# Optimization experiments

Hardware: AMD Instinct MI355X
Metric: run time of the kernel (lower is better)

## Reference

```python
import jax, jax.numpy as jnp
import numpy as np

B = 4096       # batch of query embeddings
E = 512        # embedding_size
C = 2000       # num_classes
PROXIES = 32   # imprinted weight vectors per class
P = C * PROXIES  # 64000 total stacked weight rows
EPS = 1e-12    # torch F.normalize eps


def _l2_normalize(x):
    # F.normalize(x, p=2, dim=1): divide by norm clamped to eps
    n = jnp.linalg.norm(x, axis=1, keepdims=True)
    return x / jnp.maximum(n, EPS)


def setup_inputs() -> dict:
    key = jax.random.key(0)
    k1, k2 = jax.random.split(key)
    data = jax.random.normal(k1, (B, E), dtype=jnp.float32)
    w1 = jax.random.normal(k2, (P, E), dtype=jnp.float32)
    segment_ids = jnp.arange(P, dtype=jnp.int32)  # raw row index; class id derived in reference
    return {"data": data, "w1": w1, "segment_ids": segment_ids}


def reference(data, w1, segment_ids):
    # class id of each stacked weight row (contiguous blocks, as torch vstack([*w1s]))
    seg = (segment_ids * C) // P  # == idx // PROXIES, shape [P]
    # normalize: input data at forward time; weights were l2-normalized at imprint time
    d = _l2_normalize(data)   # [B, E]
    w = _l2_normalize(w1)     # [P, E]
    # x = w1 @ data.T : per-proxy activations  [P, B]
    x = jnp.einsum('pe,be->pb', w, d)
    # per-class max over each class's ragged proxy block -> [C, B]
    y = jax.ops.segment_max(x, seg, num_segments=C)
    return y
```

## Files before the change

kernel.cpp:

```cpp
#include <hip/hip_runtime.h>

#define B_Q   4096
#define E_DIM 512
#define N_C   2000
#define N_P   64000

#define BM 128
#define BN 128

typedef int i32x4 __attribute__((ext_vector_type(4)));

__device__ __forceinline__ void async_ld16(const void* g, void* l) {
  __builtin_amdgcn_global_load_lds(
      (const __attribute__((address_space(1))) void*)g,
      (__attribute__((address_space(3))) void*)l,
      16, 0, 0);
}

__global__ __launch_bounds__(128) void normq_kernel(
    const float* __restrict__ w1, const float* __restrict__ data,
    signed char* __restrict__ wq, signed char* __restrict__ dq,
    float* __restrict__ wsc, float* __restrict__ dsc)
{
  int row = blockIdx.x;
  const float* in; signed char* outq; float* sc;
  if (row < N_P) { in = w1;   outq = wq; sc = wsc; }
  else           { in = data; outq = dq; sc = dsc; row -= N_P; }
  const int tid = threadIdx.x;
  const float4 v = *(const float4*)(in + (size_t)row * E_DIM + tid * 4);
  float ss = v.x*v.x + v.y*v.y + v.z*v.z + v.w*v.w;
  float am = fmaxf(fmaxf(fabsf(v.x), fabsf(v.y)), fmaxf(fabsf(v.z), fabsf(v.w)));
  #pragma unroll
  for (int s = 1; s < 64; s <<= 1) {
    ss += __shfl_xor(ss, s);
    am = fmaxf(am, __shfl_xor(am, s));
  }
  __shared__ float pss[2], pam[2];
  if ((tid & 63) == 0) { pss[tid >> 6] = ss; pam[tid >> 6] = am; }
  __syncthreads();
  const float inv = 1.0f / fmaxf(sqrtf(pss[0] + pss[1]), 1e-12f);
  const float m   = fmaxf(fmaxf(pam[0], pam[1]) * inv, 1e-20f);
  const float qs  = 127.0f / m * inv;
  char4 o;
  o.x = (signed char)__float2int_rn(v.x * qs);
  o.y = (signed char)__float2int_rn(v.y * qs);
  o.z = (signed char)__float2int_rn(v.z * qs);
  o.w = (signed char)__float2int_rn(v.w * qs);
  *(char4*)(outq + (size_t)row * E_DIM + tid * 4) = o;
  if (tid == 0) sc[row] = m * (1.0f / 127.0f);
}

#define WAITV(N) asm volatile("s_waitcnt vmcnt(" #N ")" ::: "memory")
#define LGKM0    asm volatile("s_waitcnt lgkmcnt(0)" ::: "memory")
#define SBAR     asm volatile("s_barrier" ::: "memory")
#define NOPS     do {} while (0)

#define STAGE_A(BUF,KOFF) do { \
  async_ld16(gA + (KOFF)*64,         smem + (BUF)*8192 + sdst); \
  async_ld16(gA + 32768 + (KOFF)*64, smem + (BUF)*8192 + sdst + 4096); \
} while(0)

#define STAGE_B(BUF,KOFF) do { \
  async_ld16(gB + (KOFF)*64,         smem + 16384 + (BUF)*8192 + sdst); \
  async_ld16(gB + 32768 + (KOFF)*64, smem + 16384 + (BUF)*8192 + sdst + 4096); \
} while(0)

#define RD(BUF) do { \
  fa0 = *(const i32x4*)(pa + (BUF)*8192 +    0); \
  fa1 = *(const i32x4*)(pa + (BUF)*8192 + 1024); \
  fa2 = *(const i32x4*)(pa + (BUF)*8192 + 2048); \
  fa3 = *(const i32x4*)(pa + (BUF)*8192 + 3072); \
  fb0 = *(const i32x4*)(pb + (BUF)*8192 +    0); \
  fb1 = *(const i32x4*)(pb + (BUF)*8192 + 1024); \
  fb2 = *(const i32x4*)(pb + (BUF)*8192 + 2048); \
  fb3 = *(const i32x4*)(pb + (BUF)*8192 + 3072); \
} while(0)

#define MM(m,n) \
  acc[m][n] = __builtin_amdgcn_mfma_i32_16x16x64_i8(fa##m, fb##n, acc[m][n], 0, 0, 0)

#define MFMA16 do { \
  MM(0,0); MM(0,1); MM(0,2); MM(0,3); \
  MM(1,0); MM(1,1); MM(1,2); MM(1,3); \
  MM(2,0); MM(2,1); MM(2,2); MM(2,3); \
  MM(3,0); MM(3,1); MM(3,2); MM(3,3); \
} while(0)

#define ITER(BUF, STAGE, WAIT) do { \
  RD(BUF); \
  LGKM0; \
  SBAR; \
  STAGE; \
  WAIT; \
  SBAR; \
  __builtin_amdgcn_s_setprio(1); \
  MFMA16; \
  __builtin_amdgcn_s_setprio(0); \
} while(0)

__global__ __launch_bounds__(256, 4) void gemm_max_kernel(
    const signed char* __restrict__ wq,
    const signed char* __restrict__ dq,
    const float* __restrict__ wsc,
    const float* __restrict__ dsc,
    float* __restrict__ out)
{
  __shared__ __align__(16) char smem[32768];

  const int tid  = threadIdx.x;
  const int lane = tid & 63;
  const int wid  = tid >> 6;
  const int wr   = wid >> 1;
  const int wc   = wid & 1;

  const int bid  = blockIdx.x;
  const int wgid = (bid & 7) * 2000 + (bid >> 3);
  const int rowb = wgid >> 5;
  const int colb = wgid & 31;
  const int rowBase = rowb * BM;
  const int colBase = colb * BN;

  const int srow = tid >> 2;
  const int gch  = (tid & 3) ^ ((tid >> 3) & 3);
  const signed char* gA = wq + (size_t)(rowBase + srow) * E_DIM + gch * 16;
  const signed char* gB = dq + (size_t)(colBase + srow) * E_DIM + gch * 16;
  const int sdst = tid * 16;

  const int r   = lane & 15;
  const int kg  = lane >> 4;
  const int swz = (kg ^ ((r >> 1) & 3)) * 16;
  const char* pa = smem + (wr * 64 + r) * 64 + swz;
  const char* pb = smem + 16384 + (wc * 64 + r) * 64 + swz;

  i32x4 acc[4][4];
  #pragma unroll
  for (int m = 0; m < 4; ++m)
    #pragma unroll
    for (int n = 0; n < 4; ++n)
      acc[m][n] = (i32x4){0, 0, 0, 0};

  i32x4 fa0, fa1, fa2, fa3, fb0, fb1, fb2, fb3;

  STAGE_A(0,0); STAGE_B(0,0);
  STAGE_A(1,1); STAGE_B(1,1);
  WAITV(4);
  SBAR;

  ITER(0, STAGE_A(0,2); STAGE_B(0,2), WAITV(4));
  ITER(1, STAGE_A(1,3); STAGE_B(1,3), WAITV(4));
  ITER(0, STAGE_A(0,4); STAGE_B(0,4), WAITV(4));
  ITER(1, STAGE_A(1,5); STAGE_B(1,5), WAITV(4));
  ITER(0, STAGE_A(0,6); STAGE_B(0,6), WAITV(4));
  ITER(1, STAGE_A(1,7); STAGE_B(1,7), WAITV(4));
  ITER(0, NOPS,                       WAITV(0));
  ITER(1, NOPS,                       NOPS);

  float wsv[4][4];
  {
    #pragma unroll
    for (int m = 0; m < 4; ++m) {
      const float4 w4 = *(const float4*)(wsc + rowBase + wr * 64 + m * 16 + kg * 4);
      wsv[m][0] = w4.x; wsv[m][1] = w4.y; wsv[m][2] = w4.z; wsv[m][3] = w4.w;
    }
  }
  float dv[4];
  {
    const float* dscp = dsc + colBase + wc * 64 + r;
    #pragma unroll
    for (int n = 0; n < 4; ++n) dv[n] = dscp[n * 16];
  }
  const int classBase = rowb * 4 + wr * 2;
  #pragma unroll
  for (int q = 0; q < 2; ++q) {
    #pragma unroll
    for (int n = 0; n < 4; ++n) {
      float pm = -3.4e38f;
      #pragma unroll
      for (int j = 0; j < 4; ++j)
        pm = fmaxf(pm, fmaxf((float)acc[2*q][n][j]   * wsv[2*q][j],
                             (float)acc[2*q+1][n][j] * wsv[2*q+1][j]));
      pm = fmaxf(pm, __shfl_xor(pm, 16));
      pm = fmaxf(pm, __shfl_xor(pm, 32));
      if (lane < 16)
        out[(size_t)(classBase + q) * B_Q + colBase + wc * 64 + n * 16 + r]
            = pm * dv[n];
    }
  }
}

extern "C" void kernel_launch(void* const* d_in, const int* in_sizes, int n_in,
                              void* d_out, int out_size, void* d_ws, size_t ws_size,
                              hipStream_t stream) {
  const float* data = (const float*)d_in[0];
  const float* w1   = (const float*)d_in[1];
  float* out = (float*)d_out;

  signed char* wq = (signed char*)d_ws;
  signed char* dq = wq + (size_t)N_P * E_DIM;
  float* wsc = (float*)(dq + (size_t)B_Q * E_DIM);
  float* dsc = wsc + N_P;

  normq_kernel<<<N_P + B_Q, 128, 0, stream>>>(w1, data, wq, dq, wsc, dsc);
  gemm_max_kernel<<<(N_P / BM) * (B_Q / BN), 256, 0, stream>>>(wq, dq, wsc, dsc, out);
}
```

Before: 185.1 us.

## Double-buffer MFMA fragments in registers and interleave LDS reads with MFMAs

The GEMM main loop now keeps two register sets of A/B fragments. The LDS reads for the next K-step are issued right after the current step's MFMAs, and sched_group_barrier directives interleave those reads with the MFMA stream, so shared-memory latency is hidden behind matrix math instead of stalling before each step. Launch bounds drop from 4 to 3 waves per SIMD to make room for the extra fragment registers. This may reduce occupancy-based latency hiding.

```diff
diff --git a/kernel.cpp b/kernel.cpp
--- a/kernel.cpp
+++ b/kernel.cpp
@@ -65,40 +65,51 @@
   async_ld16(gB + 32768 + (KOFF)*64, smem + 16384 + (BUF)*8192 + sdst + 4096); \
 } while(0)
 
-#define RD(BUF) do { \
-  fa0 = *(const i32x4*)(pa + (BUF)*8192 +    0); \
-  fa1 = *(const i32x4*)(pa + (BUF)*8192 + 1024); \
-  fa2 = *(const i32x4*)(pa + (BUF)*8192 + 2048); \
-  fa3 = *(const i32x4*)(pa + (BUF)*8192 + 3072); \
-  fb0 = *(const i32x4*)(pb + (BUF)*8192 +    0); \
-  fb1 = *(const i32x4*)(pb + (BUF)*8192 + 1024); \
-  fb2 = *(const i32x4*)(pb + (BUF)*8192 + 2048); \
-  fb3 = *(const i32x4*)(pb + (BUF)*8192 + 3072); \
-} while(0)
-
-#define MM(m,n) \
-  acc[m][n] = __builtin_amdgcn_mfma_i32_16x16x64_i8(fa##m, fb##n, acc[m][n], 0, 0, 0)
-
-#define MFMA16 do { \
-  MM(0,0); MM(0,1); MM(0,2); MM(0,3); \
-  MM(1,0); MM(1,1); MM(1,2); MM(1,3); \
-  MM(2,0); MM(2,1); MM(2,2); MM(2,3); \
-  MM(3,0); MM(3,1); MM(3,2); MM(3,3); \
-} while(0)
-
-#define ITER(BUF, STAGE, WAIT) do { \
-  RD(BUF); \
-  LGKM0; \
+#define RD(S,BUF) do { \
+  fa##S##0 = *(const i32x4*)(pa + (BUF)*8192 +    0); \
+  fa##S##1 = *(const i32x4*)(pa + (BUF)*8192 + 1024); \
+  fa##S##2 = *(const i32x4*)(pa + (BUF)*8192 + 2048); \
+  fa##S##3 = *(const i32x4*)(pa + (BUF)*8192 + 3072); \
+  fb##S##0 = *(const i32x4*)(pb + (BUF)*8192 +    0); \
+  fb##S##1 = *(const i32x4*)(pb + (BUF)*8192 + 1024); \
+  fb##S##2 = *(const i32x4*)(pb + (BUF)*8192 + 2048); \
+  fb##S##3 = *(const i32x4*)(pb + (BUF)*8192 + 3072); \
+} while(0)
+
+#define MM(S,m,n) \
+  acc[m][n] = __builtin_amdgcn_mfma_i32_16x16x64_i8(fa##S##m, fb##S##n, acc[m][n], 0, 0, 0)
+
+#define MFMA16(S) do { \
+  MM(S,0,0); MM(S,0,1); MM(S,0,2); MM(S,0,3); \
+  MM(S,1,0); MM(S,1,1); MM(S,1,2); MM(S,1,3); \
+  MM(S,2,0); MM(S,2,1); MM(S,2,2); MM(S,2,3); \
+  MM(S,3,0); MM(S,3,1); MM(S,3,2); MM(S,3,3); \
+} while(0)
+
+#define SGB(M,N) __builtin_amdgcn_sched_group_barrier(M, N, 0)
+#define ILV8 do { \
+  SGB(0x8,1); SGB(0x100,1); SGB(0x8,1); SGB(0x100,1); \
+  SGB(0x8,1); SGB(0x100,1); SGB(0x8,1); SGB(0x100,1); \
+  SGB(0x8,1); SGB(0x100,1); SGB(0x8,1); SGB(0x100,1); \
+  SGB(0x8,1); SGB(0x100,1); SGB(0x8,1); SGB(0x100,1); \
+  SGB(0x8,8); \
+} while(0)
+
+#define ITER(S,BUF, STAGE, WAIT, TAIL, ILV) do { \
   SBAR; \
   STAGE; \
   WAIT; \
   SBAR; \
+  __builtin_amdgcn_sched_barrier(0); \
   __builtin_amdgcn_s_setprio(1); \
-  MFMA16; \
+  MFMA16(S); \
+  TAIL; \
+  ILV; \
+  LGKM0; \
   __builtin_amdgcn_s_setprio(0); \
 } while(0)
 
-__global__ __launch_bounds__(256, 4) void gemm_max_kernel(
+__global__ __launch_bounds__(256, 3) void gemm_max_kernel(
     const signed char* __restrict__ wq,
     const signed char* __restrict__ dq,
     const float* __restrict__ wsc,
@@ -139,21 +150,24 @@
     for (int n = 0; n < 4; ++n)
       acc[m][n] = (i32x4){0, 0, 0, 0};
 
-  i32x4 fa0, fa1, fa2, fa3, fb0, fb1, fb2, fb3;
+  i32x4 fa00, fa01, fa02, fa03, fb00, fb01, fb02, fb03;
+  i32x4 fa10, fa11, fa12, fa13, fb10, fb11, fb12, fb13;
 
   STAGE_A(0,0); STAGE_B(0,0);
   STAGE_A(1,1); STAGE_B(1,1);
   WAITV(4);
   SBAR;
-
-  ITER(0, STAGE_A(0,2); STAGE_B(0,2), WAITV(4));
-  ITER(1, STAGE_A(1,3); STAGE_B(1,3), WAITV(4));
-  ITER(0, STAGE_A(0,4); STAGE_B(0,4), WAITV(4));
-  ITER(1, STAGE_A(1,5); STAGE_B(1,5), WAITV(4));
-  ITER(0, STAGE_A(0,6); STAGE_B(0,6), WAITV(4));
-  ITER(1, STAGE_A(1,7); STAGE_B(1,7), WAITV(4));
-  ITER(0, NOPS,                       WAITV(0));
-  ITER(1, NOPS,                       NOPS);
+  RD(0,0);
+  LGKM0;
+
+  ITER(0,0, STAGE_A(0,2); STAGE_B(0,2), WAITV(4), RD(1,1), ILV8);
+  ITER(1,1, STAGE_A(1,3); STAGE_B(1,3), WAITV(4), RD(0,0), ILV8);
+  ITER(0,0, STAGE_A(0,4); STAGE_B(0,4), WAITV(4), RD(1,1), ILV8);
+  ITER(1,1, STAGE_A(1,5); STAGE_B(1,5), WAITV(4), RD(0,0), ILV8);
+  ITER(0,0, STAGE_A(0,6); STAGE_B(0,6), WAITV(4), RD(1,1), ILV8);
+  ITER(1,1, STAGE_A(1,7); STAGE_B(1,7), WAITV(4), RD(0,0), ILV8);
+  ITER(0,0, NOPS,                       WAITV(0), RD(1,1), ILV8);
+  ITER(1,1, NOPS,                       NOPS,     NOPS,    NOPS);
 
   float wsv[4][4];
   {
```

Measured after the change: 183.4 us. Within noise of the previous version (-0.9%).

## Pre-swizzle int8 operands into MFMA fragment layout and drop LDS staging

Applied to the files above, without the earlier changes.

The quantize kernel now writes int8 weights and queries directly in the per-lane MFMA fragment order. The GEMM then loads fragments straight from global memory into registers with no shared memory or barriers. Each wave keeps its full 64-row A slice (all K) resident in registers and streams B fragments with double buffering across 8 column chunks of 64. This removes LDS traffic and synchronisation, at the cost of heavy register use (launch bounds 2) and B being reread from L2 by every wave.

```diff
diff --git a/kernel.cpp b/kernel.cpp
--- a/kernel.cpp
+++ b/kernel.cpp
@@ -5,27 +5,20 @@
 #define N_C   2000
 #define N_P   64000
 
-#define BM 128
-#define BN 128
 
 typedef int i32x4 __attribute__((ext_vector_type(4)));
 
-__device__ __forceinline__ void async_ld16(const void* g, void* l) {
-  __builtin_amdgcn_global_load_lds(
-      (const __attribute__((address_space(1))) void*)g,
-      (__attribute__((address_space(3))) void*)l,
-      16, 0, 0);
-}
-
 __global__ __launch_bounds__(128) void normq_kernel(
     const float* __restrict__ w1, const float* __restrict__ data,
-    signed char* __restrict__ wq, signed char* __restrict__ dq,
+    signed char* __restrict__ wqf, signed char* __restrict__ dqf,
     float* __restrict__ wsc, float* __restrict__ dsc)
 {
   int row = blockIdx.x;
-  const float* in; signed char* outq; float* sc;
-  if (row < N_P) { in = w1;   outq = wq; sc = wsc; }
-  else           { in = data; outq = dq; sc = dsc; row -= N_P; }
+  const bool isW = (row < N_P);
+  const float* in;
+  signed char* dst; float* sc;
+  if (isW) { in = w1;   dst = wqf; sc = wsc; }
+  else     { in = data; dst = dqf; sc = dsc; row -= N_P; }
   const int tid = threadIdx.x;
   const float4 v = *(const float4*)(in + (size_t)row * E_DIM + tid * 4);
   float ss = v.x*v.x + v.y*v.y + v.z*v.z + v.w*v.w;
@@ -46,145 +39,111 @@
   o.y = (signed char)__float2int_rn(v.y * qs);
   o.z = (signed char)__float2int_rn(v.z * qs);
   o.w = (signed char)__float2int_rn(v.w * qs);
-  *(char4*)(outq + (size_t)row * E_DIM + tid * 4) = o;
+  const int c16 = row >> 4, r = row & 15;
+  const int kt = tid >> 4, kg = (tid >> 2) & 3;
+  *(char4*)(dst + (size_t)(c16 * 8 + kt) * 1024 + (kg * 16 + r) * 16
+                + (tid & 3) * 4) = o;
   if (tid == 0) sc[row] = m * (1.0f / 127.0f);
 }
 
-#define WAITV(N) asm volatile("s_waitcnt vmcnt(" #N ")" ::: "memory")
-#define LGKM0    asm volatile("s_waitcnt lgkmcnt(0)" ::: "memory")
-#define SBAR     asm volatile("s_barrier" ::: "memory")
-#define NOPS     do {} while (0)
+#define MF(a,b,c) __builtin_amdgcn_mfma_i32_16x16x64_i8(a, b, c, 0, 0, 0)
 
-#define STAGE_A(BUF,KOFF) do { \
-  async_ld16(gA + (KOFF)*64,         smem + (BUF)*8192 + sdst); \
-  async_ld16(gA + 32768 + (KOFF)*64, smem + (BUF)*8192 + sdst + 4096); \
+#define LDB(S,OFF,KT) do { \
+  b##S##0 = *(const i32x4*)(gBc + (OFF) + (0*8+(KT))*1024); \
+  b##S##1 = *(const i32x4*)(gBc + (OFF) + (1*8+(KT))*1024); \
+  b##S##2 = *(const i32x4*)(gBc + (OFF) + (2*8+(KT))*1024); \
+  b##S##3 = *(const i32x4*)(gBc + (OFF) + (3*8+(KT))*1024); \
 } while(0)
 
-#define STAGE_B(BUF,KOFF) do { \
-  async_ld16(gB + (KOFF)*64,         smem + 16384 + (BUF)*8192 + sdst); \
-  async_ld16(gB + 32768 + (KOFF)*64, smem + 16384 + (BUF)*8192 + sdst + 4096); \
+#define MFMA_KT(S,KT) do { \
+  acc[0][0]=MF(A[0][KT],b##S##0,acc[0][0]); acc[0][1]=MF(A[0][KT],b##S##1,acc[0][1]); \
+  acc[0][2]=MF(A[0][KT],b##S##2,acc[0][2]); acc[0][3]=MF(A[0][KT],b##S##3,acc[0][3]); \
+  acc[1][0]=MF(A[1][KT],b##S##0,acc[1][0]); acc[1][1]=MF(A[1][KT],b##S##1,acc[1][1]); \
+  acc[1][2]=MF(A[1][KT],b##S##2,acc[1][2]); acc[1][3]=MF(A[1][KT],b##S##3,acc[1][3]); \
+  acc[2][0]=MF(A[2][KT],b##S##0,acc[2][0]); acc[2][1]=MF(A[2][KT],b##S##1,acc[2][1]); \
+  acc[2][2]=MF(A[2][KT],b##S##2,acc[2][2]); acc[2][3]=MF(A[2][KT],b##S##3,acc[2][3]); \
+  acc[3][0]=MF(A[3][KT],b##S##0,acc[3][0]); acc[3][1]=MF(A[3][KT],b##S##1,acc[3][1]); \
+  acc[3][2]=MF(A[3][KT],b##S##2,acc[3][2]); acc[3][3]=MF(A[3][KT],b##S##3,acc[3][3]); \
 } while(0)
 
-#define RD(BUF) do { \
-  fa0 = *(const i32x4*)(pa + (BUF)*8192 +    0); \
-  fa1 = *(const i32x4*)(pa + (BUF)*8192 + 1024); \
-  fa2 = *(const i32x4*)(pa + (BUF)*8192 + 2048); \
-  fa3 = *(const i32x4*)(pa + (BUF)*8192 + 3072); \
-  fb0 = *(const i32x4*)(pb + (BUF)*8192 +    0); \
-  fb1 = *(const i32x4*)(pb + (BUF)*8192 + 1024); \
-  fb2 = *(const i32x4*)(pb + (BUF)*8192 + 2048); \
-  fb3 = *(const i32x4*)(pb + (BUF)*8192 + 3072); \
-} while(0)
-
-#define MM(m,n) \
-  acc[m][n] = __builtin_amdgcn_mfma_i32_16x16x64_i8(fa##m, fb##n, acc[m][n], 0, 0, 0)
-
-#define MFMA16 do { \
-  MM(0,0); MM(0,1); MM(0,2); MM(0,3); \
-  MM(1,0); MM(1,1); MM(1,2); MM(1,3); \
-  MM(2,0); MM(2,1); MM(2,2); MM(2,3); \
-  MM(3,0); MM(3,1); MM(3,2); MM(3,3); \
-} while(0)
-
-#define ITER(BUF, STAGE, WAIT) do { \
-  RD(BUF); \
-  LGKM0; \
-  SBAR; \
-  STAGE; \
-  WAIT; \
-  SBAR; \
-  __builtin_amdgcn_s_setprio(1); \
-  MFMA16; \
-  __builtin_amdgcn_s_setprio(0); \
-} while(0)
-
-__global__ __launch_bounds__(256, 4) void gemm_max_kernel(
-    const signed char* __restrict__ wq,
-    const signed char* __restrict__ dq,
+__global__ __launch_bounds__(256, 2) void gemm_max_kernel(
+    const signed char* __restrict__ wqf,
+    const signed char* __restrict__ dqf,
     const float* __restrict__ wsc,
     const float* __restrict__ dsc,
     float* __restrict__ out)
 {
-  __shared__ __align__(16) char smem[32768];
-
   const int tid  = threadIdx.x;
   const int lane = tid & 63;
   const int wid  = tid >> 6;
-  const int wr   = wid >> 1;
-  const int wc   = wid & 1;
 
   const int bid  = blockIdx.x;
-  const int wgid = (bid & 7) * 2000 + (bid >> 3);
-  const int rowb = wgid >> 5;
-  const int colb = wgid & 31;
-  const int rowBase = rowb * BM;
-  const int colBase = colb * BN;
+  const int wgid = (bid & 7) * 250 + (bid >> 3);
+  const int w    = wgid * 4 + wid;
+  const int rowGroup = w >> 3;
+  const int colOct   = w & 7;
 
-  const int srow = tid >> 2;
-  const int gch  = (tid & 3) ^ ((tid >> 3) & 3);
-  const signed char* gA = wq + (size_t)(rowBase + srow) * E_DIM + gch * 16;
-  const signed char* gB = dq + (size_t)(colBase + srow) * E_DIM + gch * 16;
-  const int sdst = tid * 16;
-
-  const int r   = lane & 15;
-  const int kg  = lane >> 4;
-  const int swz = (kg ^ ((r >> 1) & 3)) * 16;
-  const char* pa = smem + (wr * 64 + r) * 64 + swz;
-  const char* pb = smem + 16384 + (wc * 64 + r) * 64 + swz;
-
-  i32x4 acc[4][4];
+  const signed char* gAp = wqf + (size_t)rowGroup * 32768 + lane * 16;
+  i32x4 A[4][8];
   #pragma unroll
   for (int m = 0; m < 4; ++m)
     #pragma unroll
-    for (int n = 0; n < 4; ++n)
-      acc[m][n] = (i32x4){0, 0, 0, 0};
+    for (int kt = 0; kt < 8; ++kt)
+      A[m][kt] = *(const i32x4*)(gAp + (m * 8 + kt) * 1024);
 
-  i32x4 fa0, fa1, fa2, fa3, fb0, fb1, fb2, fb3;
+  const signed char* gBc = dqf + (size_t)colOct * 8 * 32768 + lane * 16;
 
-  STAGE_A(0,0); STAGE_B(0,0);
-  STAGE_A(1,1); STAGE_B(1,1);
-  WAITV(4);
-  SBAR;
+  const int r  = lane & 15;
+  const int kg = lane >> 4;
 
-  ITER(0, STAGE_A(0,2); STAGE_B(0,2), WAITV(4));
-  ITER(1, STAGE_A(1,3); STAGE_B(1,3), WAITV(4));
-  ITER(0, STAGE_A(0,4); STAGE_B(0,4), WAITV(4));
-  ITER(1, STAGE_A(1,5); STAGE_B(1,5), WAITV(4));
-  ITER(0, STAGE_A(0,6); STAGE_B(0,6), WAITV(4));
-  ITER(1, STAGE_A(1,7); STAGE_B(1,7), WAITV(4));
-  ITER(0, NOPS,                       WAITV(0));
-  ITER(1, NOPS,                       NOPS);
+  i32x4 b00, b01, b02, b03, b10, b11, b12, b13;
+  i32x4 acc[4][4];
 
-  float wsv[4][4];
-  {
+  LDB(0, 0, 0);
+
+  float* outp = out + (size_t)(rowGroup * 2) * B_Q + colOct * 512;
+  const float* wscp = wsc + rowGroup * 64 + kg * 4;
+  const float* dscp = dsc + colOct * 512 + r;
+
+  #pragma unroll 1
+  for (int cc = 0; cc < 8; ++cc) {
     #pragma unroll
-    for (int m = 0; m < 4; ++m) {
-      const float4 w4 = *(const float4*)(wsc + rowBase + wr * 64 + m * 16 + kg * 4);
-      wsv[m][0] = w4.x; wsv[m][1] = w4.y; wsv[m][2] = w4.z; wsv[m][3] = w4.w;
+    for (int m = 0; m < 4; ++m)
+      #pragma unroll
+      for (int n = 0; n < 4; ++n)
+        acc[m][n] = (i32x4){0, 0, 0, 0};
+
+    LDB(1, 0, 1);       MFMA_KT(0, 0);
+    LDB(0, 0, 2);       MFMA_KT(1, 1);
+    LDB(1, 0, 3);       MFMA_KT(0, 2);
+    LDB(0, 0, 4);       MFMA_KT(1, 3);
+    LDB(1, 0, 5);       MFMA_KT(0, 4);
+    LDB(0, 0, 6);       MFMA_KT(1, 5);
+    LDB(1, 0, 7);       MFMA_KT(0, 6);
+    LDB(0, 32768, 0);   MFMA_KT(1, 7);
+
+    #pragma unroll
+    for (int q = 0; q < 2; ++q) {
+      const float4 w0 = *(const float4*)(wscp + (2*q)     * 16);
+      const float4 w1 = *(const float4*)(wscp + (2*q + 1) * 16);
+      #pragma unroll
+      for (int n = 0; n < 4; ++n) {
+        float pm = fmaxf(fmaxf((float)acc[2*q][n][0]   * w0.x,
+                               (float)acc[2*q][n][1]   * w0.y),
+                         fmaxf((float)acc[2*q][n][2]   * w0.z,
+                               (float)acc[2*q][n][3]   * w0.w));
+        pm = fmaxf(pm, fmaxf(fmaxf((float)acc[2*q+1][n][0] * w1.x,
+                                   (float)acc[2*q+1][n][1] * w1.y),
+                             fmaxf((float)acc[2*q+1][n][2] * w1.z,
+                                   (float)acc[2*q+1][n][3] * w1.w)));
+        pm = fmaxf(pm, __shfl_xor(pm, 16));
+        pm = fmaxf(pm, __shfl_xor(pm, 32));
+        if (lane < 16)
+          outp[(size_t)q * B_Q + cc * 64 + n * 16 + r]
+              = pm * dscp[cc * 64 + n * 16];
+      }
     }
-  }
-  float dv[4];
-  {
-    const float* dscp = dsc + colBase + wc * 64 + r;
-    #pragma unroll
-    for (int n = 0; n < 4; ++n) dv[n] = dscp[n * 16];
-  }
-  const int classBase = rowb * 4 + wr * 2;
-  #pragma unroll
-  for (int q = 0; q < 2; ++q) {
-    #pragma unroll
-    for (int n = 0; n < 4; ++n) {
-      float pm = -3.4e38f;
-      #pragma unroll
-      for (int j = 0; j < 4; ++j)
-        pm = fmaxf(pm, fmaxf((float)acc[2*q][n][j]   * wsv[2*q][j],
-                             (float)acc[2*q+1][n][j] * wsv[2*q+1][j]));
-      pm = fmaxf(pm, __shfl_xor(pm, 16));
-      pm = fmaxf(pm, __shfl_xor(pm, 32));
-      if (lane < 16)
-        out[(size_t)(classBase + q) * B_Q + colBase + wc * 64 + n * 16 + r]
-            = pm * dv[n];
-    }
+    gBc += 32768;
   }
 }
 
@@ -195,11 +154,11 @@
   const float* w1   = (const float*)d_in[1];
   float* out = (float*)d_out;
 
-  signed char* wq = (signed char*)d_ws;
-  signed char* dq = wq + (size_t)N_P * E_DIM;
-  float* wsc = (float*)(dq + (size_t)B_Q * E_DIM);
+  signed char* wqf = (signed char*)d_ws;
+  signed char* dqf = wqf + (size_t)N_P * E_DIM;
+  float* wsc = (float*)(dqf + (size_t)B_Q * E_DIM);
   float* dsc = wsc + N_P;
 
-  normq_kernel<<<N_P + B_Q, 128, 0, stream>>>(w1, data, wq, dq, wsc, dsc);
-  gemm_max_kernel<<<(N_P / BM) * (B_Q / BN), 256, 0, stream>>>(wq, dq, wsc, dsc, out);
+  normq_kernel<<<N_P + B_Q, 128, 0, stream>>>(w1, data, wqf, dqf, wsc, dsc);
+  gemm_max_kernel<<<2000, 256, 0, stream>>>(wqf, dqf, wsc, dsc, out);
 }
```

New measurement: 229.0 us. 23.8% more time.
